# Optimization experiments

Hardware: AMD Instinct MI355X
Metric: run time of the kernel (lower is better)

The kernel has to match this reference:

```python
import jax, jax.numpy as jnp
import numpy as np
import math

B, S, D = 1, 2048, 512
H = 8
DH = D // H
WIN = 128  # window_size
EPS = 1e-5


def _layernorm(x, g, b):
    mu = jnp.mean(x, axis=-1, keepdims=True)
    var = jnp.mean((x - mu) ** 2, axis=-1, keepdims=True)
    return (x - mu) * jax.lax.rsqrt(var + EPS) * g + b


def _local_attention(q, k, v, window_size):
    # q,k,v: [B,H,S,DH]. Faithful to F.pad + unfold: zero-padded keys
    # participate in softmax with score 0 (no masking), as in the original.
    w = window_size // 2
    W = 2 * w + 1
    kp = jnp.pad(k, ((0, 0), (0, 0), (w, w), (0, 0)))
    vp = jnp.pad(v, ((0, 0), (0, 0), (w, w), (0, 0)))
    idx = jnp.arange(q.shape[2])[:, None] + jnp.arange(W)[None, :]  # [S,W]
    k_win = kp[:, :, idx]  # [B,H,S,W,DH]
    v_win = vp[:, :, idx]  # [B,H,S,W,DH]
    scores = jnp.einsum('bhsd,bhswd->bhsw', q, k_win) / math.sqrt(q.shape[-1])
    attn = jax.nn.softmax(scores, axis=-1)
    return jnp.einsum('bhsw,bhswd->bhsd', attn, v_win)


def setup_inputs() -> dict:
    key = jax.random.key(0)
    ks = jax.random.split(key, 8)
    sc = 0.02
    return {
        'x': jax.random.normal(ks[0], (B, S, D), dtype=jnp.float32),
        'w_qkv': jax.random.normal(ks[1], (D, 3 * D), dtype=jnp.float32) * sc,
        'b_qkv': jnp.zeros((3 * D,), dtype=jnp.float32),
        'w_out': jax.random.normal(ks[2], (D, D), dtype=jnp.float32) * sc,
        'b_out': jnp.zeros((D,), dtype=jnp.float32),
        'ln_g': jnp.ones((D,), dtype=jnp.float32),
        'ln_b': jnp.zeros((D,), dtype=jnp.float32),
        'w1': jax.random.normal(ks[3], (D, 4 * D), dtype=jnp.float32) * sc,
        'b1': jnp.zeros((4 * D,), dtype=jnp.float32),
        'w2': jax.random.normal(ks[4], (4 * D, D), dtype=jnp.float32) * sc,
        'b2': jnp.zeros((D,), dtype=jnp.float32),
    }


def reference(x, w_qkv, b_qkv, w_out, b_out, ln_g, ln_b, w1, b1, w2, b2):
    residual = x
    xn = _layernorm(x, ln_g, ln_b)
    qkv = xn @ w_qkv + b_qkv                       # [B,S,3D]
    qkv = qkv.reshape(B, S, 3, H, DH)
    qkv = jnp.transpose(qkv, (2, 0, 3, 1, 4))      # [3,B,H,S,DH]
    q, k, v = qkv[0], qkv[1], qkv[2]
    attn_out = _local_attention(q, k, v, WIN)       # [B,H,S,DH]
    attn_out = jnp.transpose(attn_out, (0, 2, 1, 3)).reshape(B, S, D)
    attn_out = attn_out @ w_out + b_out
    out = residual + attn_out
    # FFN applied directly to `out` (no second norm in original)
    ffn = jax.nn.gelu(out @ w1 + b1, approximate=False) @ w2 + b2
    return out + ffn
```

## Files before the change

### kernel.cpp

```cpp
#include <hip/hip_runtime.h>
#include <math.h>

#define S_LEN 2048
#define DMODEL 512
#define NHEAD 8
#define DHEAD 64
#define LN_EPS 1e-5f

typedef __bf16 bf16;
typedef __bf16 bf16x8 __attribute__((ext_vector_type(8)));
typedef __bf16 bf16x4 __attribute__((ext_vector_type(4)));
typedef __bf16 bf16x2 __attribute__((ext_vector_type(2)));
typedef float f32x4 __attribute__((ext_vector_type(4)));

__device__ __forceinline__ float wave_reduce_sum(float x) {
#pragma unroll
  for (int off = 32; off > 0; off >>= 1) x += __shfl_xor(x, off);
  return x;
}

__global__ __launch_bounds__(256) void prep_kernel(
    const float* __restrict__ x, const float* __restrict__ ln_g,
    const float* __restrict__ ln_b, const float* __restrict__ w_qkv,
    const float* __restrict__ w_out, const float* __restrict__ w1,
    const float* __restrict__ w2, bf16* __restrict__ xn,
    bf16* __restrict__ wqkvT, bf16* __restrict__ woutT,
    bf16* __restrict__ w1T, bf16* __restrict__ w2T) {
  __shared__ float t[32][33];
  int b = blockIdx.x;
  const int tid = threadIdx.x;
  if (b < 2048) {
    const float2 v = ((const float2*)(x + (size_t)b * DMODEL))[tid];
    float s = v.x + v.y;
    float s2 = v.x * v.x + v.y * v.y;
    s = wave_reduce_sum(s);
    s2 = wave_reduce_sum(s2);
    __shared__ float red[2][4];
    const int wv = tid >> 6, ln = tid & 63;
    if (ln == 0) { red[0][wv] = s; red[1][wv] = s2; }
    __syncthreads();
    s = red[0][0] + red[0][1] + red[0][2] + red[0][3];
    s2 = red[1][0] + red[1][1] + red[1][2] + red[1][3];
    const float mu = s * (1.0f / DMODEL);
    const float var = s2 * (1.0f / DMODEL) - mu * mu;
    const float rs = rsqrtf(var + LN_EPS);
    const float2 gg = ((const float2*)ln_g)[tid];
    const float2 bb = ((const float2*)ln_b)[tid];
    bf16x2 o;
    o[0] = (bf16)((v.x - mu) * rs * gg.x + bb.x);
    o[1] = (bf16)((v.y - mu) * rs * gg.y + bb.y);
    ((bf16x2*)(xn + (size_t)b * DMODEL))[tid] = o;
    return;
  }
  b -= 2048;
  const float* W; bf16* WT; int K, N, bx, by;
  if (b < 768)       { W = w_qkv; WT = wqkvT; K = 512;  N = 1536; bx = b % 48; by = b / 48; }
  else if (b < 1024) { b -= 768;  W = w_out; WT = woutT; K = 512;  N = 512;  bx = b % 16; by = b / 16; }
  else if (b < 2048) { b -= 1024; W = w1;    WT = w1T;   K = 512;  N = 2048; bx = b % 64; by = b / 64; }
  else               { b -= 2048; W = w2;    WT = w2T;   K = 2048; N = 512;  bx = b % 16; by = b / 16; }
  const int c = tid & 31, r8 = tid >> 5;
  const int n0 = bx * 32, k0 = by * 32;
#pragma unroll
  for (int it = 0; it < 4; it++) {
    const int r = r8 + it * 8;
    t[r][c] = W[(size_t)(k0 + r) * N + n0 + c];
  }
  __syncthreads();
#pragma unroll
  for (int it = 0; it < 4; it++) {
    const int r = r8 + it * 8;
    WT[(size_t)(n0 + r) * K + k0 + c] = (bf16)t[c][r];
  }
}

template <int MODE>
__device__ __forceinline__ void epilogue_store(float v, const float* res,
                                               float* Cf, bf16* Cb,
                                               size_t row, size_t col, int N) {
  if (MODE == 2) v = 0.5f * v * (1.0f + erff(v * 0.70710678118654752f));
  if (MODE == 1 || MODE == 3) v += res[row * N + col];
  if (MODE == 1 || MODE == 3) Cf[row * N + col] = v;
  if (MODE == 1 || MODE == 2) Cb[row * N + col] = (bf16)v;
}

template <int MODE>
__global__ __launch_bounds__(256) void mmC_kernel(const bf16* __restrict__ A,
                                                  const bf16* __restrict__ BT,
                                                  const float* __restrict__ bias,
                                                  bf16* __restrict__ Cb,
                                                  bf16* __restrict__ vT,
                                                  int N, int K) {
  __shared__ bf16 As[2][64 * 64];
  __shared__ bf16 Bs[2][64 * 64];
  const int tid = threadIdx.x;
  const int wave = tid >> 6, lane = tid & 63;
  const int lr = lane & 15, kg = lane >> 4;
  const int wm = wave & 1, wn = wave >> 1;
  const int rowBase = blockIdx.y * 64, colBase = blockIdx.x * 64;

  const bf16* aP[2]; const bf16* bP[2]; int aOff[2], bOff[2];
#pragma unroll
  for (int r = 0; r < 2; ++r) {
    const int c = wave * 2 + r;
    const int elem = c * 512 + lane * 8;
    const int s = elem >> 11, row = (elem >> 5) & 63, kp = elem & 31;
    aP[r] = A + (size_t)(rowBase + row) * K + s * 32 + kp;
    bP[r] = BT + (size_t)(colBase + row) * K + s * 32 + kp;
    aOff[r] = c * 512;
    bOff[r] = c * 512;
  }

  auto stage = [&](int kk, int buf) {
#pragma unroll
    for (int r = 0; r < 2; ++r) {
      __builtin_amdgcn_global_load_lds(
          (const __attribute__((address_space(1))) void*)(aP[r] + kk),
          (__attribute__((address_space(3))) void*)(&As[buf][aOff[r]]), 16, 0, 0);
      __builtin_amdgcn_global_load_lds(
          (const __attribute__((address_space(1))) void*)(bP[r] + kk),
          (__attribute__((address_space(3))) void*)(&Bs[buf][bOff[r]]), 16, 0, 0);
    }
  };

  f32x4 acc[2][2] = {};
  const int niter = K >> 6;

  stage(0, 0);
  for (int it = 0; it < niter; ++it) {
    const int cur = it & 1;
    __syncthreads();
    if (it + 1 < niter) stage((it + 1) << 6, cur ^ 1);
    const bf16* as = As[cur];
    const bf16* bs = Bs[cur];
#pragma unroll
    for (int s = 0; s < 2; ++s) {
      bf16x8 af[2], bfr[2];
#pragma unroll
      for (int i = 0; i < 2; ++i)
        af[i] = *(const bf16x8*)(as + s * 2048 + (wm * 32 + i * 16 + lr) * 32 + kg * 8);
#pragma unroll
      for (int j = 0; j < 2; ++j)
        bfr[j] = *(const bf16x8*)(bs + s * 2048 + (wn * 32 + j * 16 + lr) * 32 + kg * 8);
#pragma unroll
      for (int i = 0; i < 2; ++i)
#pragma unroll
        for (int j = 0; j < 2; ++j)
          acc[i][j] = __builtin_amdgcn_mfma_f32_16x16x32_bf16(af[i], bfr[j],
                                                              acc[i][j], 0, 0, 0);
    }
  }

#pragma unroll
  for (int j = 0; j < 2; ++j) {
    const int col = colBase + wn * 32 + j * 16 + lr;
    const float bs = bias[col];
    if (MODE == 4 && col >= 1024) {
      bf16* dst = vT + (size_t)(col - 1024) * S_LEN;
#pragma unroll
      for (int i = 0; i < 2; ++i) {
        bf16x4 p;
#pragma unroll
        for (int r = 0; r < 4; ++r) p[r] = (bf16)(acc[i][j][r] + bs);
        *(bf16x4*)(dst + rowBase + wm * 32 + i * 16 + kg * 4) = p;
      }
    } else {
#pragma unroll
      for (int i = 0; i < 2; ++i)
#pragma unroll
        for (int r = 0; r < 4; ++r) {
          const size_t row = rowBase + wm * 32 + i * 16 + kg * 4 + r;
          float v = acc[i][j][r] + bs;
          if (MODE == 2) v = 0.5f * v * (1.0f + erff(v * 0.70710678118654752f));
          Cb[row * N + col] = (bf16)v;
        }
    }
  }
}

template <int MODE>
__global__ __launch_bounds__(256) void mmB_kernel(const bf16* __restrict__ A,
                                                  const bf16* __restrict__ BT,
                                                  const float* __restrict__ bias,
                                                  const float* __restrict__ res,
                                                  float* __restrict__ Cf,
                                                  bf16* __restrict__ Cb,
                                                  int N, int K) {
  __shared__ bf16 As[2][32 * 64];
  __shared__ bf16 Bs[2][64 * 64];
  const int tid = threadIdx.x;
  const int wave = tid >> 6, lane = tid & 63;
  const int lr = lane & 15, kg = lane >> 4;
  const int rowBase = blockIdx.y * 32, colBase = blockIdx.x * 64;

  const bf16* aP; const bf16* bP[2]; int aOff, bOff[2];
  {
    const int elem = wave * 512 + lane * 8;
    const int s = elem >> 10, row = (elem >> 5) & 31, kp = elem & 31;
    aP = A + (size_t)(rowBase + row) * K + s * 32 + kp;
    aOff = wave * 512;
  }
#pragma unroll
  for (int r = 0; r < 2; ++r) {
    const int c = wave * 2 + r;
    const int elem = c * 512 + lane * 8;
    const int s = elem >> 11, row = (elem >> 5) & 63, kp = elem & 31;
    bP[r] = BT + (size_t)(colBase + row) * K + s * 32 + kp;
    bOff[r] = c * 512;
  }

  auto stage = [&](int kk, int buf) {
    __builtin_amdgcn_global_load_lds(
        (const __attribute__((address_space(1))) void*)(aP + kk),
        (__attribute__((address_space(3))) void*)(&As[buf][aOff]), 16, 0, 0);
#pragma unroll
    for (int r = 0; r < 2; ++r)
      __builtin_amdgcn_global_load_lds(
          (const __attribute__((address_space(1))) void*)(bP[r] + kk),
          (__attribute__((address_space(3))) void*)(&Bs[buf][bOff[r]]), 16, 0, 0);
  };

  f32x4 acc[2] = {};
  const int niter = K >> 6;

  stage(0, 0);
  for (int it = 0; it < niter; ++it) {
    const int cur = it & 1;
    __syncthreads();
    if (it + 1 < niter) stage((it + 1) << 6, cur ^ 1);
    const bf16* as = As[cur];
    const bf16* bs = Bs[cur];
#pragma unroll
    for (int s = 0; s < 2; ++s) {
      bf16x8 af[2], bfr;
#pragma unroll
      for (int i = 0; i < 2; ++i)
        af[i] = *(const bf16x8*)(as + s * 1024 + (i * 16 + lr) * 32 + kg * 8);
      bfr = *(const bf16x8*)(bs + s * 2048 + (wave * 16 + lr) * 32 + kg * 8);
#pragma unroll
      for (int i = 0; i < 2; ++i)
        acc[i] = __builtin_amdgcn_mfma_f32_16x16x32_bf16(af[i], bfr, acc[i], 0, 0, 0);
    }
  }

  {
    const int col = colBase + wave * 16 + lr;
    const float bs = bias[col];
#pragma unroll
    for (int i = 0; i < 2; ++i)
#pragma unroll
      for (int r = 0; r < 4; ++r)
        epilogue_store<MODE>(acc[i][r] + bs, res, Cf, Cb,
                             (size_t)(rowBase + i * 16 + kg * 4 + r),
                             (size_t)col, N);
  }
}

__global__ __launch_bounds__(256) void attn_fused(const bf16* __restrict__ qkvb,
                                                  const bf16* __restrict__ vT,
                                                  bf16* __restrict__ attnb) {
  __shared__ bf16 Kl[192][72];
  __shared__ bf16 Vt[64][200];
  __shared__ bf16 Ql[64][72];

  const int tid = threadIdx.x;
  const int s0 = blockIdx.x * 64;
  const int hc = blockIdx.y * DHEAD;

  {
    const int row = tid >> 2, c0 = (tid & 3) * 16;
    const bf16* src = qkvb + (size_t)(s0 + row) * 1536 + hc + c0;
    *(bf16x8*)&Ql[row][c0] = *(const bf16x8*)src;
    *(bf16x8*)&Ql[row][c0 + 8] = *(const bf16x8*)(src + 8);
  }
#pragma unroll
  for (int it = 0; it < 3; it++) {
    const int row = it * 64 + (tid >> 2), c0 = (tid & 3) * 16;
    const int p = s0 - 64 + row;
    bf16x8 a, b;
    if (p >= 0 && p < S_LEN) {
      const bf16* src = qkvb + (size_t)p * 1536 + 512 + hc + c0;
      a = *(const bf16x8*)src;
      b = *(const bf16x8*)(src + 8);
    } else {
#pragma unroll
      for (int j = 0; j < 8; j++) { a[j] = (bf16)0.f; b[j] = (bf16)0.f; }
    }
    *(bf16x8*)&Kl[row][c0] = a;
    *(bf16x8*)&Kl[row][c0 + 8] = b;
  }
  {
    const int d = tid >> 2, r0 = (tid & 3) * 48;
    const bf16* src = vT + (size_t)(hc + d) * S_LEN;
#pragma unroll
    for (int i = 0; i < 6; i++) {
      const int p0 = s0 - 64 + r0 + i * 8;
      bf16x8 v;
      if (p0 >= 0 && p0 + 8 <= S_LEN) {
        v = *(const bf16x8*)(src + p0);
      } else {
#pragma unroll
        for (int j = 0; j < 8; j++) {
          const int p = p0 + j;
          v[j] = (p >= 0 && p < S_LEN) ? src[p] : (bf16)0.f;
        }
      }
      *(bf16x8*)&Vt[d][r0 + i * 8] = v;
    }
  }
  __syncthreads();

  const int wv = tid >> 6, lane = tid & 63;
  const int lr = lane & 15, kg = lane >> 4;

  f32x4 c[12] = {};
#pragma unroll
  for (int step = 0; step < 2; step++) {
    const bf16x8 qf = *(const bf16x8*)&Ql[wv * 16 + lr][step * 32 + kg * 8];
#pragma unroll
    for (int t = 0; t < 12; t++) {
      const bf16x8 kf = *(const bf16x8*)&Kl[t * 16 + lr][step * 32 + kg * 8];
      c[t] = __builtin_amdgcn_mfma_f32_16x16x32_bf16(qf, kf, c[t], 0, 0, 0);
    }
  }

  float e[12][4];
  float inv[4];
#pragma unroll
  for (int rr = 0; rr < 4; rr++) {
    const int q = wv * 16 + kg * 4 + rr;
    float m = -1e30f;
#pragma unroll
    for (int t = 0; t < 12; t++) {
      const int col = t * 16 + lr;
      if (col >= q && col <= q + 128) m = fmaxf(m, c[t][rr] * 0.125f);
    }
#pragma unroll
    for (int off = 1; off < 16; off <<= 1) m = fmaxf(m, __shfl_xor(m, off));
    float sum = 0.f;
#pragma unroll
    for (int t = 0; t < 12; t++) {
      const int col = t * 16 + lr;
      const bool valid = (col >= q) && (col <= q + 128);
      const float ev = valid ? __expf(c[t][rr] * 0.125f - m) : 0.f;
      e[t][rr] = ev;
      sum += ev;
    }
#pragma unroll
    for (int off = 1; off < 16; off <<= 1) sum += __shfl_xor(sum, off);
    inv[rr] = 1.f / sum;
  }

  __syncthreads();

  bf16* Pl = (bf16*)Kl + wv * (16 * 200);
#pragma unroll
  for (int rr = 0; rr < 4; rr++)
#pragma unroll
    for (int t = 0; t < 12; t++)
      Pl[(kg * 4 + rr) * 200 + t * 16 + lr] = (bf16)(e[t][rr] * inv[rr]);

  f32x4 o[4] = {};
#pragma unroll
  for (int step = 0; step < 6; step++) {
    const bf16x8 pf = *(const bf16x8*)&Pl[lr * 200 + step * 32 + kg * 8];
#pragma unroll
    for (int jt = 0; jt < 4; jt++) {
      const bf16x8 vf = *(const bf16x8*)&Vt[jt * 16 + lr][step * 32 + kg * 8];
      o[jt] = __builtin_amdgcn_mfma_f32_16x16x32_bf16(pf, vf, o[jt], 0, 0, 0);
    }
  }

#pragma unroll
  for (int jt = 0; jt < 4; jt++)
#pragma unroll
    for (int rr = 0; rr < 4; rr++) {
      const int q = wv * 16 + kg * 4 + rr;
      attnb[(size_t)(s0 + q) * DMODEL + hc + jt * 16 + lr] = (bf16)o[jt][rr];
    }
}

extern "C" void kernel_launch(void* const* d_in, const int* in_sizes, int n_in,
                              void* d_out, int out_size, void* d_ws, size_t ws_size,
                              hipStream_t stream) {
  const float* x     = (const float*)d_in[0];
  const float* w_qkv = (const float*)d_in[1];
  const float* b_qkv = (const float*)d_in[2];
  const float* w_out = (const float*)d_in[3];
  const float* b_out = (const float*)d_in[4];
  const float* ln_g  = (const float*)d_in[5];
  const float* ln_b  = (const float*)d_in[6];
  const float* w1    = (const float*)d_in[7];
  const float* b1    = (const float*)d_in[8];
  const float* w2    = (const float*)d_in[9];
  const float* b2    = (const float*)d_in[10];
  float* out = (float*)d_out;

  char* w = (char*)d_ws;
  const size_t MB = 1u << 20;
  bf16* xn    = (bf16*)(w + 0);
  bf16* attnb = (bf16*)(w + 0);
  bf16* qkvb  = (bf16*)(w + 2 * MB);
  bf16* outb  = (bf16*)(w + 2 * MB);
  bf16* vT    = (bf16*)(w + 8 * MB);
  bf16* h1    = (bf16*)(w + 10 * MB);
  bf16* wqkvT = (bf16*)(w + 18 * MB);
  bf16* woutT = (bf16*)(w + 19 * MB + 512 * 1024);
  bf16* w1T   = (bf16*)(w + 20 * MB);
  bf16* w2T   = (bf16*)(w + 22 * MB);

  prep_kernel<<<5120, 256, 0, stream>>>(x, ln_g, ln_b, w_qkv, w_out, w1, w2,
                                        xn, wqkvT, woutT, w1T, w2T);
  mmC_kernel<4><<<dim3(24, 32), 256, 0, stream>>>(xn, wqkvT, b_qkv, qkvb, vT,
                                                  1536, 512);
  attn_fused<<<dim3(32, 8), 256, 0, stream>>>(qkvb, vT, attnb);
  mmB_kernel<1><<<dim3(8, 64), 256, 0, stream>>>(attnb, woutT, b_out, x, out,
                                                 outb, 512, 512);
  mmC_kernel<2><<<dim3(32, 32), 256, 0, stream>>>(outb, w1T, b1, h1, nullptr,
                                                  2048, 512);
  mmB_kernel<3><<<dim3(8, 64), 256, 0, stream>>>(h1, w2T, b2, out, out,
                                                 nullptr, 512, 2048);
}
```

Measured before the change: 141.6 us.

## Overlap weight transposes with QKV GEMM and split-K the second FFN GEMM

The prep kernel now handles only layernorm and the QKV weight transpose. The transposes of the out-projection, W1 and W2 weights move into extra blocks of the QKV GEMM launch, so they run alongside the GEMM tiles instead of ahead of them. The final FFN GEMM (K=2048) is split into two K halves that accumulate into the residual output with float atomics, doubling the block count to 1024 for better CU occupancy. This adds atomic traffic and makes the summation order nondeterministic.

```diff
diff --git a/kernel.cpp b/kernel.cpp
--- a/kernel.cpp
+++ b/kernel.cpp
@@ -19,14 +19,31 @@
   return x;
 }
 
-__global__ __launch_bounds__(256) void prep_kernel(
+__device__ __forceinline__ void transpose_tile(const float* __restrict__ W,
+                                               bf16* __restrict__ WT, int K,
+                                               int N, int bx, int by,
+                                               float (*t)[33], int tid) {
+  const int c = tid & 31, r8 = tid >> 5;
+  const int n0 = bx * 32, k0 = by * 32;
+#pragma unroll
+  for (int it = 0; it < 4; it++) {
+    const int r = r8 + it * 8;
+    t[r][c] = W[(size_t)(k0 + r) * N + n0 + c];
+  }
+  __syncthreads();
+#pragma unroll
+  for (int it = 0; it < 4; it++) {
+    const int r = r8 + it * 8;
+    WT[(size_t)(n0 + r) * K + k0 + c] = (bf16)t[c][r];
+  }
+}
+
+__global__ __launch_bounds__(256) void prep1_kernel(
     const float* __restrict__ x, const float* __restrict__ ln_g,
     const float* __restrict__ ln_b, const float* __restrict__ w_qkv,
-    const float* __restrict__ w_out, const float* __restrict__ w1,
-    const float* __restrict__ w2, bf16* __restrict__ xn,
-    bf16* __restrict__ wqkvT, bf16* __restrict__ woutT,
-    bf16* __restrict__ w1T, bf16* __restrict__ w2T) {
+    bf16* __restrict__ xn, bf16* __restrict__ wqkvT) {
   __shared__ float t[32][33];
+  __shared__ float red[2][4];
   int b = blockIdx.x;
   const int tid = threadIdx.x;
   if (b < 2048) {
@@ -35,7 +52,6 @@
     float s2 = v.x * v.x + v.y * v.y;
     s = wave_reduce_sum(s);
     s2 = wave_reduce_sum(s2);
-    __shared__ float red[2][4];
     const int wv = tid >> 6, ln = tid & 63;
     if (ln == 0) { red[0][wv] = s; red[1][wv] = s2; }
     __syncthreads();
@@ -53,43 +69,113 @@
     return;
   }
   b -= 2048;
-  const float* W; bf16* WT; int K, N, bx, by;
-  if (b < 768)       { W = w_qkv; WT = wqkvT; K = 512;  N = 1536; bx = b % 48; by = b / 48; }
-  else if (b < 1024) { b -= 768;  W = w_out; WT = woutT; K = 512;  N = 512;  bx = b % 16; by = b / 16; }
-  else if (b < 2048) { b -= 1024; W = w1;    WT = w1T;   K = 512;  N = 2048; bx = b % 64; by = b / 64; }
-  else               { b -= 2048; W = w2;    WT = w2T;   K = 2048; N = 512;  bx = b % 16; by = b / 16; }
-  const int c = tid & 31, r8 = tid >> 5;
-  const int n0 = bx * 32, k0 = by * 32;
-#pragma unroll
-  for (int it = 0; it < 4; it++) {
-    const int r = r8 + it * 8;
-    t[r][c] = W[(size_t)(k0 + r) * N + n0 + c];
-  }
-  __syncthreads();
-#pragma unroll
-  for (int it = 0; it < 4; it++) {
-    const int r = r8 + it * 8;
-    WT[(size_t)(n0 + r) * K + k0 + c] = (bf16)t[c][r];
-  }
-}
-
-template <int MODE>
-__device__ __forceinline__ void epilogue_store(float v, const float* res,
-                                               float* Cf, bf16* Cb,
-                                               size_t row, size_t col, int N) {
-  if (MODE == 2) v = 0.5f * v * (1.0f + erff(v * 0.70710678118654752f));
-  if (MODE == 1 || MODE == 3) v += res[row * N + col];
-  if (MODE == 1 || MODE == 3) Cf[row * N + col] = v;
-  if (MODE == 1 || MODE == 2) Cb[row * N + col] = (bf16)v;
-}
-
-template <int MODE>
-__global__ __launch_bounds__(256) void mmC_kernel(const bf16* __restrict__ A,
-                                                  const bf16* __restrict__ BT,
-                                                  const float* __restrict__ bias,
-                                                  bf16* __restrict__ Cb,
-                                                  bf16* __restrict__ vT,
-                                                  int N, int K) {
+  transpose_tile(w_qkv, wqkvT, 512, 1536, b % 48, b / 48, t, tid);
+}
+
+__global__ __launch_bounds__(256) void qkv_pack(
+    const bf16* __restrict__ A, const bf16* __restrict__ BT,
+    const float* __restrict__ bias, bf16* __restrict__ qkvb,
+    bf16* __restrict__ vT, const float* __restrict__ w_out,
+    const float* __restrict__ w1, const float* __restrict__ w2,
+    bf16* __restrict__ woutT, bf16* __restrict__ w1T, bf16* __restrict__ w2T) {
+  __shared__ bf16 As[2][64 * 64];
+  __shared__ bf16 Bs[2][64 * 64];
+  int b = blockIdx.x;
+  const int tid = threadIdx.x;
+
+  if (b >= 768) {
+    b -= 768;
+    float(*t)[33] = (float(*)[33])As;
+    if (b < 256)       transpose_tile(w_out, woutT, 512, 512, b % 16, b / 16, t, tid);
+    else if (b < 1280) { b -= 256;  transpose_tile(w1, w1T, 512, 2048, b % 64, b / 64, t, tid); }
+    else               { b -= 1280; transpose_tile(w2, w2T, 2048, 512, b % 16, b / 16, t, tid); }
+    return;
+  }
+
+  const int K = 512, N = 1536;
+  const int wave = tid >> 6, lane = tid & 63;
+  const int lr = lane & 15, kg = lane >> 4;
+  const int wm = wave & 1, wn = wave >> 1;
+  const int rowBase = (b / 24) * 64, colBase = (b % 24) * 64;
+
+  const bf16* aP[2]; const bf16* bP[2]; int off[2];
+#pragma unroll
+  for (int r = 0; r < 2; ++r) {
+    const int c = wave * 2 + r;
+    const int elem = c * 512 + lane * 8;
+    const int s = elem >> 11, row = (elem >> 5) & 63, kp = elem & 31;
+    aP[r] = A + (size_t)(rowBase + row) * K + s * 32 + kp;
+    bP[r] = BT + (size_t)(colBase + row) * K + s * 32 + kp;
+    off[r] = c * 512;
+  }
+  auto stage = [&](int kk, int buf) {
+#pragma unroll
+    for (int r = 0; r < 2; ++r) {
+      __builtin_amdgcn_global_load_lds(
+          (const __attribute__((address_space(1))) void*)(aP[r] + kk),
+          (__attribute__((address_space(3))) void*)(&As[buf][off[r]]), 16, 0, 0);
+      __builtin_amdgcn_global_load_lds(
+          (const __attribute__((address_space(1))) void*)(bP[r] + kk),
+          (__attribute__((address_space(3))) void*)(&Bs[buf][off[r]]), 16, 0, 0);
+    }
+  };
+
+  f32x4 acc[2][2] = {};
+  stage(0, 0);
+  for (int it = 0; it < 8; ++it) {
+    const int cur = it & 1;
+    __syncthreads();
+    if (it < 7) stage((it + 1) << 6, cur ^ 1);
+    const bf16* as = As[cur];
+    const bf16* bs = Bs[cur];
+#pragma unroll
+    for (int s = 0; s < 2; ++s) {
+      bf16x8 af[2], bfr[2];
+#pragma unroll
+      for (int i = 0; i < 2; ++i)
+        af[i] = *(const bf16x8*)(as + s * 2048 + (wm * 32 + i * 16 + lr) * 32 + kg * 8);
+#pragma unroll
+      for (int j = 0; j < 2; ++j)
+        bfr[j] = *(const bf16x8*)(bs + s * 2048 + (wn * 32 + j * 16 + lr) * 32 + kg * 8);
+#pragma unroll
+      for (int i = 0; i < 2; ++i)
+#pragma unroll
+        for (int j = 0; j < 2; ++j)
+          acc[i][j] = __builtin_amdgcn_mfma_f32_16x16x32_bf16(af[i], bfr[j],
+                                                              acc[i][j], 0, 0, 0);
+    }
+  }
+
+#pragma unroll
+  for (int j = 0; j < 2; ++j) {
+    const int col = colBase + wn * 32 + j * 16 + lr;
+    const float bs = bias[col];
+    if (col >= 1024) {
+      bf16* dst = vT + (size_t)(col - 1024) * S_LEN;
+#pragma unroll
+      for (int i = 0; i < 2; ++i) {
+        bf16x4 p;
+#pragma unroll
+        for (int r = 0; r < 4; ++r) p[r] = (bf16)(acc[i][j][r] + bs);
+        *(bf16x4*)(dst + rowBase + wm * 32 + i * 16 + kg * 4) = p;
+      }
+    } else {
+#pragma unroll
+      for (int i = 0; i < 2; ++i)
+#pragma unroll
+        for (int r = 0; r < 4; ++r) {
+          const size_t row = rowBase + wm * 32 + i * 16 + kg * 4 + r;
+          qkvb[row * N + col] = (bf16)(acc[i][j][r] + bs);
+        }
+    }
+  }
+}
+
+__global__ __launch_bounds__(256) void mmC_gelu(const bf16* __restrict__ A,
+                                                const bf16* __restrict__ BT,
+                                                const float* __restrict__ bias,
+                                                bf16* __restrict__ Cb,
+                                                int N, int K) {
   __shared__ bf16 As[2][64 * 64];
   __shared__ bf16 Bs[2][64 * 64];
   const int tid = threadIdx.x;
@@ -98,7 +184,7 @@
   const int wm = wave & 1, wn = wave >> 1;
   const int rowBase = blockIdx.y * 64, colBase = blockIdx.x * 64;
 
-  const bf16* aP[2]; const bf16* bP[2]; int aOff[2], bOff[2];
+  const bf16* aP[2]; const bf16* bP[2]; int off[2];
 #pragma unroll
   for (int r = 0; r < 2; ++r) {
     const int c = wave * 2 + r;
@@ -106,25 +192,22 @@
     const int s = elem >> 11, row = (elem >> 5) & 63, kp = elem & 31;
     aP[r] = A + (size_t)(rowBase + row) * K + s * 32 + kp;
     bP[r] = BT + (size_t)(colBase + row) * K + s * 32 + kp;
-    aOff[r] = c * 512;
-    bOff[r] = c * 512;
-  }
-
+    off[r] = c * 512;
+  }
   auto stage = [&](int kk, int buf) {
 #pragma unroll
     for (int r = 0; r < 2; ++r) {
       __builtin_amdgcn_global_load_lds(
           (const __attribute__((address_space(1))) void*)(aP[r] + kk),
-          (__attribute__((address_space(3))) void*)(&As[buf][aOff[r]]), 16, 0, 0);
+          (__attribute__((address_space(3))) void*)(&As[buf][off[r]]), 16, 0, 0);
       __builtin_amdgcn_global_load_lds(
           (const __attribute__((address_space(1))) void*)(bP[r] + kk),
-          (__attribute__((address_space(3))) void*)(&Bs[buf][bOff[r]]), 16, 0, 0);
+          (__attribute__((address_space(3))) void*)(&Bs[buf][off[r]]), 16, 0, 0);
     }
   };
 
   f32x4 acc[2][2] = {};
   const int niter = K >> 6;
-
   stage(0, 0);
   for (int it = 0; it < niter; ++it) {
     const int cur = it & 1;
@@ -154,37 +237,23 @@
   for (int j = 0; j < 2; ++j) {
     const int col = colBase + wn * 32 + j * 16 + lr;
     const float bs = bias[col];
-    if (MODE == 4 && col >= 1024) {
-      bf16* dst = vT + (size_t)(col - 1024) * S_LEN;
-#pragma unroll
-      for (int i = 0; i < 2; ++i) {
-        bf16x4 p;
-#pragma unroll
-        for (int r = 0; r < 4; ++r) p[r] = (bf16)(acc[i][j][r] + bs);
-        *(bf16x4*)(dst + rowBase + wm * 32 + i * 16 + kg * 4) = p;
+#pragma unroll
+    for (int i = 0; i < 2; ++i)
+#pragma unroll
+      for (int r = 0; r < 4; ++r) {
+        const size_t row = rowBase + wm * 32 + i * 16 + kg * 4 + r;
+        float v = acc[i][j][r] + bs;
+        v = 0.5f * v * (1.0f + erff(v * 0.70710678118654752f));
+        Cb[row * N + col] = (bf16)v;
       }
-    } else {
-#pragma unroll
-      for (int i = 0; i < 2; ++i)
-#pragma unroll
-        for (int r = 0; r < 4; ++r) {
-          const size_t row = rowBase + wm * 32 + i * 16 + kg * 4 + r;
-          float v = acc[i][j][r] + bs;
-          if (MODE == 2) v = 0.5f * v * (1.0f + erff(v * 0.70710678118654752f));
-          Cb[row * N + col] = (bf16)v;
-        }
-    }
-  }
-}
-
-template <int MODE>
-__global__ __launch_bounds__(256) void mmB_kernel(const bf16* __restrict__ A,
-                                                  const bf16* __restrict__ BT,
-                                                  const float* __restrict__ bias,
-                                                  const float* __restrict__ res,
-                                                  float* __restrict__ Cf,
-                                                  bf16* __restrict__ Cb,
-                                                  int N, int K) {
+  }
+}
+
+__global__ __launch_bounds__(256) void outproj_kernel(
+    const bf16* __restrict__ A, const bf16* __restrict__ BT,
+    const float* __restrict__ bias, const float* __restrict__ res,
+    float* __restrict__ Cf, bf16* __restrict__ Cb) {
+  const int N = 512, K = 512;
   __shared__ bf16 As[2][32 * 64];
   __shared__ bf16 Bs[2][64 * 64];
   const int tid = threadIdx.x;
@@ -207,7 +276,6 @@
     bP[r] = BT + (size_t)(colBase + row) * K + s * 32 + kp;
     bOff[r] = c * 512;
   }
-
   auto stage = [&](int kk, int buf) {
     __builtin_amdgcn_global_load_lds(
         (const __attribute__((address_space(1))) void*)(aP + kk),
@@ -220,13 +288,11 @@
   };
 
   f32x4 acc[2] = {};
-  const int niter = K >> 6;
-
   stage(0, 0);
-  for (int it = 0; it < niter; ++it) {
+  for (int it = 0; it < 8; ++it) {
     const int cur = it & 1;
     __syncthreads();
-    if (it + 1 < niter) stage((it + 1) << 6, cur ^ 1);
+    if (it < 7) stage((it + 1) << 6, cur ^ 1);
     const bf16* as = As[cur];
     const bf16* bs = Bs[cur];
 #pragma unroll
@@ -248,10 +314,88 @@
 #pragma unroll
     for (int i = 0; i < 2; ++i)
 #pragma unroll
-      for (int r = 0; r < 4; ++r)
-        epilogue_store<MODE>(acc[i][r] + bs, res, Cf, Cb,
-                             (size_t)(rowBase + i * 16 + kg * 4 + r),
-                             (size_t)col, N);
+      for (int r = 0; r < 4; ++r) {
+        const size_t row = rowBase + i * 16 + kg * 4 + r;
+        const float v = acc[i][r] + bs + res[row * N + col];
+        Cf[row * N + col] = v;
+        Cb[row * N + col] = (bf16)v;
+      }
+  }
+}
+
+__global__ __launch_bounds__(256) void ffn2_splitk(const bf16* __restrict__ A,
+                                                   const bf16* __restrict__ BT,
+                                                   const float* __restrict__ bias,
+                                                   float* __restrict__ out) {
+  const int N = 512, K = 2048;
+  __shared__ bf16 As[2][32 * 64];
+  __shared__ bf16 Bs[2][64 * 64];
+  const int b = blockIdx.x;
+  const int kh = b & 1;
+  const int tile = b >> 1;
+  const int tid = threadIdx.x;
+  const int wave = tid >> 6, lane = tid & 63;
+  const int lr = lane & 15, kg = lane >> 4;
+  const int rowBase = (tile >> 3) * 32, colBase = (tile & 7) * 64;
+  const int kBase = kh * 1024;
+
+  const bf16* aP; const bf16* bP[2]; int aOff, bOff[2];
+  {
+    const int elem = wave * 512 + lane * 8;
+    const int s = elem >> 10, row = (elem >> 5) & 31, kp = elem & 31;
+    aP = A + (size_t)(rowBase + row) * K + kBase + s * 32 + kp;
+    aOff = wave * 512;
+  }
+#pragma unroll
+  for (int r = 0; r < 2; ++r) {
+    const int c = wave * 2 + r;
+    const int elem = c * 512 + lane * 8;
+    const int s = elem >> 11, row = (elem >> 5) & 63, kp = elem & 31;
+    bP[r] = BT + (size_t)(colBase + row) * K + kBase + s * 32 + kp;
+    bOff[r] = c * 512;
+  }
+  auto stage = [&](int kk, int buf) {
+    __builtin_amdgcn_global_load_lds(
+        (const __attribute__((address_space(1))) void*)(aP + kk),
+        (__attribute__((address_space(3))) void*)(&As[buf][aOff]), 16, 0, 0);
+#pragma unroll
+    for (int r = 0; r < 2; ++r)
+      __builtin_amdgcn_global_load_lds(
+          (const __attribute__((address_space(1))) void*)(bP[r] + kk),
+          (__attribute__((address_space(3))) void*)(&Bs[buf][bOff[r]]), 16, 0, 0);
+  };
+
+  f32x4 acc[2] = {};
+  stage(0, 0);
+  for (int it = 0; it < 16; ++it) {
+    const int cur = it & 1;
+    __syncthreads();
+    if (it < 15) stage((it + 1) << 6, cur ^ 1);
+    const bf16* as = As[cur];
+    const bf16* bs = Bs[cur];
+#pragma unroll
+    for (int s = 0; s < 2; ++s) {
+      bf16x8 af[2], bfr;
+#pragma unroll
+      for (int i = 0; i < 2; ++i)
+        af[i] = *(const bf16x8*)(as + s * 1024 + (i * 16 + lr) * 32 + kg * 8);
+      bfr = *(const bf16x8*)(bs + s * 2048 + (wave * 16 + lr) * 32 + kg * 8);
+#pragma unroll
+      for (int i = 0; i < 2; ++i)
+        acc[i] = __builtin_amdgcn_mfma_f32_16x16x32_bf16(af[i], bfr, acc[i], 0, 0, 0);
+    }
+  }
+
+  {
+    const int col = colBase + wave * 16 + lr;
+    const float bs = (kh == 0) ? bias[col] : 0.0f;
+#pragma unroll
+    for (int i = 0; i < 2; ++i)
+#pragma unroll
+      for (int r = 0; r < 4; ++r) {
+        const size_t row = rowBase + i * 16 + kg * 4 + r;
+        unsafeAtomicAdd(&out[row * N + col], acc[i][r] + bs);
+      }
   }
 }
 
@@ -408,15 +552,12 @@
   bf16* w1T   = (bf16*)(w + 20 * MB);
   bf16* w2T   = (bf16*)(w + 22 * MB);
 
-  prep_kernel<<<5120, 256, 0, stream>>>(x, ln_g, ln_b, w_qkv, w_out, w1, w2,
-                                        xn, wqkvT, woutT, w1T, w2T);
-  mmC_kernel<4><<<dim3(24, 32), 256, 0, stream>>>(xn, wqkvT, b_qkv, qkvb, vT,
-                                                  1536, 512);
+  prep1_kernel<<<2816, 256, 0, stream>>>(x, ln_g, ln_b, w_qkv, xn, wqkvT);
+  qkv_pack<<<3072, 256, 0, stream>>>(xn, wqkvT, b_qkv, qkvb, vT,
+                                     w_out, w1, w2, woutT, w1T, w2T);
   attn_fused<<<dim3(32, 8), 256, 0, stream>>>(qkvb, vT, attnb);
-  mmB_kernel<1><<<dim3(8, 64), 256, 0, stream>>>(attnb, woutT, b_out, x, out,
-                                                 outb, 512, 512);
-  mmC_kernel<2><<<dim3(32, 32), 256, 0, stream>>>(outb, w1T, b1, h1, nullptr,
-                                                  2048, 512);
-  mmB_kernel<3><<<dim3(8, 64), 256, 0, stream>>>(h1, w2T, b2, out, out,
-                                                 nullptr, 512, 2048);
-}
+  outproj_kernel<<<dim3(8, 64), 256, 0, stream>>>(attnb, woutT, b_out, x, out,
+                                                  outb);
+  mmC_gelu<<<dim3(32, 32), 256, 0, stream>>>(outb, w1T, b1, h1, 2048, 512);
+  ffn2_splitk<<<1024, 256, 0, stream>>>(h1, w2T, b2, out);
+}
```

Measured after the change: 143.2 us. About the same (+1.1%).

## Split-K FFN down-projection with atomic accumulation and LDS-staged coalesced stores

Applied to the files above, without the earlier changes.

The final FFN GEMM (K=2048) moves from 32x64 tiles over the full K to the 64x64 mmC kernel with a two-way split of K. Each half adds its partial result into the fp32 output, which already holds the residual, using atomic adds; only the first half adds the bias. The mmC epilogue for the bf16 outputs now stages the tile in LDS and writes 16-byte vectors per row, replacing scattered 2-byte stores. The intent is more MFMA work per load and better-coalesced writes, at the cost of fp32 atomic traffic and non-deterministic summation order.

```diff
diff --git a/kernel.cpp b/kernel.cpp
--- a/kernel.cpp
+++ b/kernel.cpp
@@ -73,58 +73,51 @@
   }
 }
 
-template <int MODE>
-__device__ __forceinline__ void epilogue_store(float v, const float* res,
-                                               float* Cf, bf16* Cb,
-                                               size_t row, size_t col, int N) {
-  if (MODE == 2) v = 0.5f * v * (1.0f + erff(v * 0.70710678118654752f));
-  if (MODE == 1 || MODE == 3) v += res[row * N + col];
-  if (MODE == 1 || MODE == 3) Cf[row * N + col] = v;
-  if (MODE == 1 || MODE == 2) Cb[row * N + col] = (bf16)v;
-}
-
-template <int MODE>
+template <int MODE, int SPLITK>
 __global__ __launch_bounds__(256) void mmC_kernel(const bf16* __restrict__ A,
                                                   const bf16* __restrict__ BT,
                                                   const float* __restrict__ bias,
                                                   bf16* __restrict__ Cb,
                                                   bf16* __restrict__ vT,
-                                                  int N, int K) {
+                                                  float* __restrict__ outF,
+                                                  int N, int K, int gx) {
   __shared__ bf16 As[2][64 * 64];
   __shared__ bf16 Bs[2][64 * 64];
   const int tid = threadIdx.x;
+  int b = blockIdx.x;
+  int kh = 0;
+  if (SPLITK > 0) { kh = b & 1; b >>= 1; }
   const int wave = tid >> 6, lane = tid & 63;
   const int lr = lane & 15, kg = lane >> 4;
   const int wm = wave & 1, wn = wave >> 1;
-  const int rowBase = blockIdx.y * 64, colBase = blockIdx.x * 64;
-
-  const bf16* aP[2]; const bf16* bP[2]; int aOff[2], bOff[2];
+  const int rowBase = (b / gx) * 64, colBase = (b % gx) * 64;
+  const int ldk = (SPLITK > 0) ? 2 * SPLITK : K;
+  const int kBase = kh * ((SPLITK > 0) ? SPLITK : 0);
+
+  const bf16* aP[2]; const bf16* bP[2]; int off[2];
 #pragma unroll
   for (int r = 0; r < 2; ++r) {
     const int c = wave * 2 + r;
     const int elem = c * 512 + lane * 8;
     const int s = elem >> 11, row = (elem >> 5) & 63, kp = elem & 31;
-    aP[r] = A + (size_t)(rowBase + row) * K + s * 32 + kp;
-    bP[r] = BT + (size_t)(colBase + row) * K + s * 32 + kp;
-    aOff[r] = c * 512;
-    bOff[r] = c * 512;
-  }
-
+    aP[r] = A + (size_t)(rowBase + row) * ldk + kBase + s * 32 + kp;
+    bP[r] = BT + (size_t)(colBase + row) * ldk + kBase + s * 32 + kp;
+    off[r] = c * 512;
+  }
   auto stage = [&](int kk, int buf) {
 #pragma unroll
     for (int r = 0; r < 2; ++r) {
       __builtin_amdgcn_global_load_lds(
           (const __attribute__((address_space(1))) void*)(aP[r] + kk),
-          (__attribute__((address_space(3))) void*)(&As[buf][aOff[r]]), 16, 0, 0);
+          (__attribute__((address_space(3))) void*)(&As[buf][off[r]]), 16, 0, 0);
       __builtin_amdgcn_global_load_lds(
           (const __attribute__((address_space(1))) void*)(bP[r] + kk),
-          (__attribute__((address_space(3))) void*)(&Bs[buf][bOff[r]]), 16, 0, 0);
+          (__attribute__((address_space(3))) void*)(&Bs[buf][off[r]]), 16, 0, 0);
     }
   };
 
   f32x4 acc[2][2] = {};
   const int niter = K >> 6;
-
   stage(0, 0);
   for (int it = 0; it < niter; ++it) {
     const int cur = it & 1;
@@ -150,11 +143,27 @@
     }
   }
 
-#pragma unroll
-  for (int j = 0; j < 2; ++j) {
-    const int col = colBase + wn * 32 + j * 16 + lr;
-    const float bs = bias[col];
-    if (MODE == 4 && col >= 1024) {
+  if (SPLITK > 0) {
+#pragma unroll
+    for (int j = 0; j < 2; ++j) {
+      const int col = colBase + wn * 32 + j * 16 + lr;
+      const float bs = (kh == 0) ? bias[col] : 0.0f;
+#pragma unroll
+      for (int i = 0; i < 2; ++i)
+#pragma unroll
+        for (int r = 0; r < 4; ++r) {
+          const size_t row = rowBase + wm * 32 + i * 16 + kg * 4 + r;
+          unsafeAtomicAdd(&outF[row * N + col], acc[i][j][r] + bs);
+        }
+    }
+    return;
+  }
+
+  if (MODE == 4 && colBase >= 1024) {
+#pragma unroll
+    for (int j = 0; j < 2; ++j) {
+      const int col = colBase + wn * 32 + j * 16 + lr;
+      const float bs = bias[col];
       bf16* dst = vT + (size_t)(col - 1024) * S_LEN;
 #pragma unroll
       for (int i = 0; i < 2; ++i) {
@@ -163,21 +172,37 @@
         for (int r = 0; r < 4; ++r) p[r] = (bf16)(acc[i][j][r] + bs);
         *(bf16x4*)(dst + rowBase + wm * 32 + i * 16 + kg * 4) = p;
       }
-    } else {
-#pragma unroll
-      for (int i = 0; i < 2; ++i)
-#pragma unroll
-        for (int r = 0; r < 4; ++r) {
-          const size_t row = rowBase + wm * 32 + i * 16 + kg * 4 + r;
-          float v = acc[i][j][r] + bs;
-          if (MODE == 2) v = 0.5f * v * (1.0f + erff(v * 0.70710678118654752f));
-          Cb[row * N + col] = (bf16)v;
-        }
-    }
-  }
-}
-
-template <int MODE>
+    }
+    return;
+  }
+
+  __syncthreads();
+  bf16* Cs = (bf16*)As;
+#pragma unroll
+  for (int j = 0; j < 2; ++j) {
+    const int colL = wn * 32 + j * 16 + lr;
+    const float bs = bias[colBase + colL];
+#pragma unroll
+    for (int i = 0; i < 2; ++i)
+#pragma unroll
+      for (int r = 0; r < 4; ++r) {
+        const int rowL = wm * 32 + i * 16 + kg * 4 + r;
+        float v = acc[i][j][r] + bs;
+        if (MODE == 2) v = 0.5f * v * (1.0f + erff(v * 0.70710678118654752f));
+        Cs[rowL * 64 + colL] = (bf16)v;
+      }
+  }
+  __syncthreads();
+  {
+    const int rowOut = tid >> 2, colOut = (tid & 3) * 16;
+    const bf16x8 v0 = *(const bf16x8*)&Cs[rowOut * 64 + colOut];
+    const bf16x8 v1 = *(const bf16x8*)&Cs[rowOut * 64 + colOut + 8];
+    bf16* dst = Cb + (size_t)(rowBase + rowOut) * N + colBase + colOut;
+    *(bf16x8*)dst = v0;
+    *(bf16x8*)(dst + 8) = v1;
+  }
+}
+
 __global__ __launch_bounds__(256) void mmB_kernel(const bf16* __restrict__ A,
                                                   const bf16* __restrict__ BT,
                                                   const float* __restrict__ bias,
@@ -207,7 +232,6 @@
     bP[r] = BT + (size_t)(colBase + row) * K + s * 32 + kp;
     bOff[r] = c * 512;
   }
-
   auto stage = [&](int kk, int buf) {
     __builtin_amdgcn_global_load_lds(
         (const __attribute__((address_space(1))) void*)(aP + kk),
@@ -221,7 +245,6 @@
 
   f32x4 acc[2] = {};
   const int niter = K >> 6;
-
   stage(0, 0);
   for (int it = 0; it < niter; ++it) {
     const int cur = it & 1;
@@ -248,10 +271,12 @@
 #pragma unroll
     for (int i = 0; i < 2; ++i)
 #pragma unroll
-      for (int r = 0; r < 4; ++r)
-        epilogue_store<MODE>(acc[i][r] + bs, res, Cf, Cb,
-                             (size_t)(rowBase + i * 16 + kg * 4 + r),
-                             (size_t)col, N);
+      for (int r = 0; r < 4; ++r) {
+        const size_t row = rowBase + i * 16 + kg * 4 + r;
+        const float v = acc[i][r] + bs + res[row * N + col];
+        Cf[row * N + col] = v;
+        Cb[row * N + col] = (bf16)v;
+      }
   }
 }
 
@@ -410,13 +435,13 @@
 
   prep_kernel<<<5120, 256, 0, stream>>>(x, ln_g, ln_b, w_qkv, w_out, w1, w2,
                                         xn, wqkvT, woutT, w1T, w2T);
-  mmC_kernel<4><<<dim3(24, 32), 256, 0, stream>>>(xn, wqkvT, b_qkv, qkvb, vT,
-                                                  1536, 512);
+  mmC_kernel<4, 0><<<768, 256, 0, stream>>>(xn, wqkvT, b_qkv, qkvb, vT,
+                                            nullptr, 1536, 512, 24);
   attn_fused<<<dim3(32, 8), 256, 0, stream>>>(qkvb, vT, attnb);
-  mmB_kernel<1><<<dim3(8, 64), 256, 0, stream>>>(attnb, woutT, b_out, x, out,
-                                                 outb, 512, 512);
-  mmC_kernel<2><<<dim3(32, 32), 256, 0, stream>>>(outb, w1T, b1, h1, nullptr,
-                                                  2048, 512);
-  mmB_kernel<3><<<dim3(8, 64), 256, 0, stream>>>(h1, w2T, b2, out, out,
-                                                 nullptr, 512, 2048);
-}
+  mmB_kernel<<<dim3(8, 64), 256, 0, stream>>>(attnb, woutT, b_out, x, out,
+                                              outb, 512, 512);
+  mmC_kernel<2, 0><<<1024, 256, 0, stream>>>(outb, w1T, b1, h1, nullptr,
+                                             nullptr, 2048, 512, 32);
+  mmC_kernel<2, 1024><<<512, 256, 0, stream>>>(h1, w2T, b2, nullptr, nullptr,
+                                               out, 512, 1024, 8);
+}
```

New measurement: 140.3 us (median of 2 runs). Within noise of the previous version (-1.0%).
